# Kernel tuning notes

Measured on AMD Instinct MI355X. Metric: run time of the kernel, lower is better.

## Reference

```python
import jax, jax.numpy as jnp
import numpy as np

INTER = 32  # inter_channels = in_channels // 2


def conv1x1(x, w, b):
    # x: (b, c_in, h, w), w: (c_out, c_in), b: (c_out,)
    return jnp.einsum('bchw,oc->bohw', x, w) + b[None, :, None, None]


def setup_inputs() -> dict:
    key = jax.random.key(0)
    ks = jax.random.split(key, 12)
    B, C, H, W = 8, 64, 64, 64
    inter = INTER
    s_in = 1.0 / np.sqrt(C)      # torch conv default init scale
    s_int = 1.0 / np.sqrt(inter)
    return {
        'x': jax.random.normal(ks[0], (B, C, H, W), jnp.float32),
        'g_w': jax.random.normal(ks[1], (inter, C), jnp.float32) * s_in,
        'g_b': jax.random.normal(ks[2], (inter,), jnp.float32) * s_in,
        'theta_w': jax.random.normal(ks[3], (inter, C), jnp.float32) * s_in,
        'theta_b': jax.random.normal(ks[4], (inter,), jnp.float32) * s_in,
        'phi_w': jax.random.normal(ks[5], (inter, C), jnp.float32) * s_in,
        'phi_b': jax.random.normal(ks[6], (inter,), jnp.float32) * s_in,
        'W_w': jax.random.normal(ks[7], (C, inter), jnp.float32) * s_int,
        'W_b': jax.random.normal(ks[8], (C,), jnp.float32) * s_int,
        'Wz1_w': jax.random.normal(ks[9], (C, inter), jnp.float32) * s_int,
        'Wz1_b': jax.random.normal(ks[10], (C,), jnp.float32) * s_int,
        'mb': jax.random.normal(ks[11], (inter, 256), jnp.float32),
    }


def reference(x, g_w, g_b, theta_w, theta_b, phi_w, phi_b, W_w, W_b, Wz1_w, Wz1_b, mb):
    b, c, h, w = x.shape
    inter = g_w.shape[0]
    # 1x1 conv projections, flattened over spatial: N = h*w
    g_x = conv1x1(x, g_w, g_b).reshape(b, inter, -1)          # (b, ic, N)
    theta_x = conv1x1(x, theta_w, theta_b).reshape(b, inter, -1)
    phi_x = conv1x1(x, phi_w, phi_b).reshape(b, inter, -1)    # (b, ic, N)
    # non-local self-attention: f = theta^T @ phi, unscaled softmax
    f = jnp.einsum('bcn,bcm->bnm', theta_x, phi_x)            # (b, N, N)
    f_div_C = jax.nn.softmax(f, axis=-1)
    y = jnp.einsum('bnm,bcm->bcn', f_div_C, g_x)              # (b, ic, N)
    y = y.reshape(b, inter, h, w)
    W_y = conv1x1(y, W_w, W_b)                                # (b, c, h, w)
    # memory-bank cross-attention: phi^T @ mb, scaled softmax
    f1 = jnp.einsum('bcn,ck->bnk', phi_x, mb)                 # (b, N, 256)
    scale = jnp.float32(int(inter) ** (-0.5))
    f_div_C1 = jax.nn.softmax(f1 * scale, axis=-1)
    y1 = jnp.einsum('bnk,ck->bcn', f_div_C1, mb)              # (b, ic, N)
    y1 = y1.reshape(b, inter, h, w)
    W_y1 = conv1x1(y1, Wz1_w, Wz1_b)
    return W_y + x + W_y1
```

## Files before the change

### kernel.cpp

```cpp
#include <hip/hip_runtime.h>
#include <hip/hip_bf16.h>

#define N_POS 4096
#define C_IN 64
#define IC 32
#define L2E 1.4426950408889634f

typedef float f32x16 __attribute__((ext_vector_type(16)));
typedef short bf16x8 __attribute__((ext_vector_type(8)));
typedef unsigned int uint;
typedef uint uint4v __attribute__((ext_vector_type(4)));
typedef unsigned short ushort;

static __device__ __forceinline__ ushort f2bf(float f) {
    __hip_bfloat16 h = __float2bfloat16(f);
    return __builtin_bit_cast(ushort, h);
}
static __device__ __forceinline__ uint packbf2(float lo, float hi) {
    return (uint)f2bf(lo) | ((uint)f2bf(hi) << 16);
}
static __device__ __forceinline__ uint packtrunc(float lo, float hi) {
    return __builtin_amdgcn_perm(__builtin_bit_cast(uint, hi),
                                 __builtin_bit_cast(uint, lo), 0x07060302u);
}

__global__ __launch_bounds__(128) void proj_kernel(
    const float* __restrict__ x,
    const float* __restrict__ g_w, const float* __restrict__ g_b,
    const float* __restrict__ th_w, const float* __restrict__ th_b,
    const float* __restrict__ ph_w, const float* __restrict__ ph_b,
    const float* __restrict__ mb,
    ushort* __restrict__ gcn, ushort* __restrict__ tht, ushort* __restrict__ pht,
    ushort* __restrict__ mbt, ushort* __restrict__ mbb)
{
    int gy = blockIdx.y;
    int pj = gy >> 2, q8 = gy & 3;
    const float* wsrc = (pj == 0) ? g_w : (pj == 1) ? th_w : ph_w;
    const float* bsrc = (pj == 0) ? g_b : (pj == 1) ? th_b : ph_b;
    __shared__ float w[8][64];
    __shared__ float bias[8];
    int tid = threadIdx.x;
    for (int i = tid; i < 512; i += 128) w[i >> 6][i & 63] = wsrc[q8 * 512 + i];
    if (tid < 8) bias[tid] = bsrc[q8 * 8 + tid];
    __syncthreads();

    int ng = blockIdx.x * 128 + tid;
    int b = ng >> 12, n = ng & 4095;
    const float* xb = x + (size_t)b * C_IN * N_POS + n;
    float xr[64];
    #pragma unroll
    for (int c = 0; c < 64; c++) xr[c] = xb[(size_t)c * N_POS];

    float acc[8];
    #pragma unroll
    for (int o = 0; o < 8; o++) {
        float a = bias[o];
        const float4* w4 = (const float4*)w[o];
        #pragma unroll
        for (int c4 = 0; c4 < 16; c4++) {
            float4 wv = w4[c4];
            a += wv.x * xr[c4*4+0] + wv.y * xr[c4*4+1]
               + wv.z * xr[c4*4+2] + wv.w * xr[c4*4+3];
        }
        if (pj == 1) a *= L2E;
        acc[o] = a;
    }

    if (pj == 0) {
        #pragma unroll
        for (int c = 0; c < 8; c++)
            gcn[((size_t)(b * IC + q8 * 8 + c)) * N_POS + n] = f2bf(acc[c]);
    } else {
        ushort* dst = ((pj == 1) ? tht : pht) + ((size_t)(b * N_POS + n)) * IC + q8 * 8;
        uint4v pk;
        #pragma unroll
        for (int i = 0; i < 4; i++) pk[i] = packbf2(acc[2*i], acc[2*i+1]);
        *(uint4v*)dst = pk;
    }

    if (gy == 0 && blockIdx.x < 64) {
        int i = blockIdx.x * 128 + tid;
        int c = i >> 8, k = i & 255;
        float v = mb[i];
        mbb[i] = f2bf(v);
        mbt[k * 32 + c] = f2bf(v * (0.17677669529663687f * L2E));
    }
}

__global__ __launch_bounds__(512) void attn_fused(
    const ushort* __restrict__ tht, const ushort* __restrict__ pht,
    const ushort* __restrict__ gcn, const ushort* __restrict__ mbt,
    const ushort* __restrict__ mbb, const float* __restrict__ x,
    const float* __restrict__ Ww, const float* __restrict__ Wb,
    const float* __restrict__ Wzw, const float* __restrict__ Wzb,
    float* __restrict__ out)
{
    __shared__ float redY[4][2][32][36];
    __shared__ float redD[8][2][32];
    __shared__ float ly1p[4][32][36];
    __shared__ float sumeL[4][32];

    int tid = threadIdx.x;
    int s = tid >> 6, lane = tid & 63;
    int bid = blockIdx.x;
    int b = bid & 7;
    int qp = bid >> 3;
    int q0 = qp * 64;
    int mbase = s * 512;
    int cl = lane & 31, h = lane >> 5;
    int t4 = (cl >> 2) & 3;
    int pcl = (t4 == 1 || t4 == 2) ? (cl ^ 12) : cl;

    const ushort* thpA = tht + ((size_t)(b * N_POS + q0 + cl)) * IC + 8 * h;
    bf16x8 thA0 = *(const bf16x8*)thpA;
    bf16x8 thA1 = *(const bf16x8*)(thpA + 16);
    const ushort* thpB = thpA + 32 * IC;
    bf16x8 thB0 = *(const bf16x8*)thpB;
    bf16x8 thB1 = *(const bf16x8*)(thpB + 16);

    const ushort* phbase = pht + (size_t)b * N_POS * IC;
    const ushort* gbase  = gcn + ((size_t)(b * IC + cl)) * N_POS;

    f32x16 yA, yB, zero;
    #pragma unroll
    for (int i = 0; i < 16; i++) { yA[i] = 0.f; yB[i] = 0.f; zero[i] = 0.f; }
    float sA0 = 0.f, sA1 = 0.f, sB0 = 0.f, sB1 = 0.f;

    #pragma unroll 2
    for (int mt = 0; mt < 16; ++mt) {
        int m0 = mbase + mt * 32;
        const ushort* php = phbase + ((size_t)(m0 + pcl)) * IC + 8 * h;
        bf16x8 ph0 = *(const bf16x8*)php;
        bf16x8 ph1 = *(const bf16x8*)(php + 16);
        const ushort* gp = gbase + m0 + 8 * h;
        bf16x8 g0 = *(const bf16x8*)gp;
        bf16x8 g1 = *(const bf16x8*)(gp + 16);

        f32x16 sv = __builtin_amdgcn_mfma_f32_32x32x16_bf16(ph0, thA0, zero, 0, 0, 0);
        sv = __builtin_amdgcn_mfma_f32_32x32x16_bf16(ph1, thA1, sv, 0, 0, 0);
        uint wA[8];
        #pragma unroll
        for (int i = 0; i < 8; i++) {
            float p0 = __builtin_amdgcn_exp2f(sv[2*i]);
            float p1 = __builtin_amdgcn_exp2f(sv[2*i+1]);
            if (i & 1) sA1 += p0 + p1; else sA0 += p0 + p1;
            wA[i] = packtrunc(p0, p1);
        }
        f32x16 sw = __builtin_amdgcn_mfma_f32_32x32x16_bf16(ph0, thB0, zero, 0, 0, 0);
        sw = __builtin_amdgcn_mfma_f32_32x32x16_bf16(ph1, thB1, sw, 0, 0, 0);
        uint wB[8];
        #pragma unroll
        for (int i = 0; i < 8; i++) {
            float p0 = __builtin_amdgcn_exp2f(sw[2*i]);
            float p1 = __builtin_amdgcn_exp2f(sw[2*i+1]);
            if (i & 1) sB1 += p0 + p1; else sB0 += p0 + p1;
            wB[i] = packtrunc(p0, p1);
        }

        uint4v aA0, aA1, aB0, aB1;
        aA0[0] = wA[0]; aA0[1] = wA[1]; aA0[2] = wA[2]; aA0[3] = wA[3];
        aA1[0] = wA[4]; aA1[1] = wA[5]; aA1[2] = wA[6]; aA1[3] = wA[7];
        aB0[0] = wB[0]; aB0[1] = wB[1]; aB0[2] = wB[2]; aB0[3] = wB[3];
        aB1[0] = wB[4]; aB1[1] = wB[5]; aB1[2] = wB[6]; aB1[3] = wB[7];

        yA = __builtin_amdgcn_mfma_f32_32x32x16_bf16(
            __builtin_bit_cast(bf16x8, aA0), g0, yA, 0, 0, 0);
        yB = __builtin_amdgcn_mfma_f32_32x32x16_bf16(
            __builtin_bit_cast(bf16x8, aB0), g0, yB, 0, 0, 0);
        yA = __builtin_amdgcn_mfma_f32_32x32x16_bf16(
            __builtin_bit_cast(bf16x8, aA1), g1, yA, 0, 0, 0);
        yB = __builtin_amdgcn_mfma_f32_32x32x16_bf16(
            __builtin_bit_cast(bf16x8, aB1), g1, yB, 0, 0, 0);
    }

    float sumeA = sA0 + sA1;
    float sumeB = sB0 + sB1;

    sumeA += __shfl_xor(sumeA, 32);
    sumeB += __shfl_xor(sumeB, 32);
    if (lane < 32) { redD[s][0][cl] = sumeA; redD[s][1][cl] = sumeB; }
    if (s < 4) {
        #pragma unroll
        for (int r = 0; r < 16; r++) {
            int q = (r & 3) + 8 * (r >> 2) + 4 * h;
            redY[s][0][q][cl] = yA[r];
            redY[s][1][q][cl] = yB[r];
        }
    }
    __syncthreads();

    if (s >= 4) {
        int sl = s - 4;
        #pragma unroll
        for (int r = 0; r < 16; r++) {
            int q = (r & 3) + 8 * (r >> 2) + 4 * h;
            redY[sl][0][q][cl] += yA[r];
            redY[sl][1][q][cl] += yB[r];
        }
    } else {
        int j = s & 1, kh = s >> 1;
        int mq0 = q0 + j * 32;
        const ushort* php = pht + ((size_t)(b * N_POS + mq0 + cl)) * IC + 8 * h;
        bf16x8 qf0 = *(const bf16x8*)php;
        bf16x8 qf1 = *(const bf16x8*)(php + 16);

        yA = zero;
        yB = zero;
        float su0 = 0.f, su1 = 0.f;

        #pragma unroll
        for (int kt = 0; kt < 4; ++kt) {
            int k0 = (kh * 4 + kt) * 32;
            const ushort* ap = mbt + ((size_t)(k0 + pcl)) * IC + 8 * h;
            bf16x8 af0 = *(const bf16x8*)ap;
            bf16x8 af1 = *(const bf16x8*)(ap + 16);
            const ushort* bp = mbb + (size_t)cl * 256 + k0 + 8 * h;
            bf16x8 bf0 = *(const bf16x8*)bp;
            bf16x8 bf1 = *(const bf16x8*)(bp + 16);

            f32x16 sv = __builtin_amdgcn_mfma_f32_32x32x16_bf16(af0, qf0, zero, 0, 0, 0);
            sv = __builtin_amdgcn_mfma_f32_32x32x16_bf16(af1, qf1, sv, 0, 0, 0);

            uint w[8];
            #pragma unroll
            for (int i = 0; i < 8; i++) {
                float p0 = __builtin_amdgcn_exp2f(sv[2*i]);
                float p1 = __builtin_amdgcn_exp2f(sv[2*i+1]);
                if (i & 1) su1 += p0 + p1; else su0 += p0 + p1;
                w[i] = packtrunc(p0, p1);
            }
            uint4v a0, a1;
            a0[0] = w[0]; a0[1] = w[1]; a0[2] = w[2]; a0[3] = w[3];
            a1[0] = w[4]; a1[1] = w[5]; a1[2] = w[6]; a1[3] = w[7];

            yA = __builtin_amdgcn_mfma_f32_32x32x16_bf16(
                __builtin_bit_cast(bf16x8, a0), bf0, yA, 0, 0, 0);
            yB = __builtin_amdgcn_mfma_f32_32x32x16_bf16(
                __builtin_bit_cast(bf16x8, a1), bf1, yB, 0, 0, 0);
        }

        float sume = su0 + su1;
        sume += __shfl_xor(sume, 32);
        if (lane < 32) sumeL[s][cl] = sume;
        #pragma unroll
        for (int r = 0; r < 16; r++) {
            int q = (r & 3) + 8 * (r >> 2) + 4 * h;
            ly1p[s][q][cl] = yA[r] + yB[r];
        }
    }
    __syncthreads();

    int nl = lane, og = s;
    int n = q0 + nl;
    int jo = nl >> 5, qo = nl & 31;

    float den = 0.f;
    #pragma unroll
    for (int s8 = 0; s8 < 8; s8++) den += redD[s8][jo][qo];
    float inv = 1.f / den;
    float inv1 = 1.f / (sumeL[jo][qo] + sumeL[2 + jo][qo]);

    float yv[32], y1v[32];
    #pragma unroll
    for (int c4 = 0; c4 < 8; c4++) {
        float4 v0 = *(const float4*)&redY[0][jo][qo][c4 * 4];
        float4 v1 = *(const float4*)&redY[1][jo][qo][c4 * 4];
        float4 v2 = *(const float4*)&redY[2][jo][qo][c4 * 4];
        float4 v3 = *(const float4*)&redY[3][jo][qo][c4 * 4];
        yv[c4*4+0] = (v0.x + v1.x + v2.x + v3.x) * inv;
        yv[c4*4+1] = (v0.y + v1.y + v2.y + v3.y) * inv;
        yv[c4*4+2] = (v0.z + v1.z + v2.z + v3.z) * inv;
        yv[c4*4+3] = (v0.w + v1.w + v2.w + v3.w) * inv;
        float4 p0 = *(const float4*)&ly1p[jo][qo][c4 * 4];
        float4 p1 = *(const float4*)&ly1p[2 + jo][qo][c4 * 4];
        y1v[c4*4+0] = (p0.x + p1.x) * inv1;
        y1v[c4*4+1] = (p0.y + p1.y) * inv1;
        y1v[c4*4+2] = (p0.z + p1.z) * inv1;
        y1v[c4*4+3] = (p0.w + p1.w) * inv1;
    }

    int obase = og * 8;
    const float* xb = x   + ((size_t)(b * C_IN + obase)) * N_POS + n;
    float*       ob = out + ((size_t)(b * C_IN + obase)) * N_POS + n;
    #pragma unroll
    for (int o = 0; o < 8; o++) {
        float acc = Wb[obase + o] + Wzb[obase + o] + xb[(size_t)o * N_POS];
        const float4* w4  = (const float4*)(Ww  + (obase + o) * 32);
        const float4* wz4 = (const float4*)(Wzw + (obase + o) * 32);
        #pragma unroll
        for (int c4 = 0; c4 < 8; c4++) {
            float4 a = w4[c4], z = wz4[c4];
            acc += a.x * yv[c4*4+0] + a.y * yv[c4*4+1] + a.z * yv[c4*4+2] + a.w * yv[c4*4+3];
            acc += z.x * y1v[c4*4+0] + z.y * y1v[c4*4+1] + z.z * y1v[c4*4+2] + z.w * y1v[c4*4+3];
        }
        ob[(size_t)o * N_POS] = acc;
    }
}

extern "C" void kernel_launch(void* const* d_in, const int* in_sizes, int n_in,
                              void* d_out, int out_size, void* d_ws, size_t ws_size,
                              hipStream_t stream) {
    const float* x    = (const float*)d_in[0];
    const float* g_w  = (const float*)d_in[1];
    const float* g_b  = (const float*)d_in[2];
    const float* th_w = (const float*)d_in[3];
    const float* th_b = (const float*)d_in[4];
    const float* ph_w = (const float*)d_in[5];
    const float* ph_b = (const float*)d_in[6];
    const float* W_w  = (const float*)d_in[7];
    const float* W_b  = (const float*)d_in[8];
    const float* Wz_w = (const float*)d_in[9];
    const float* Wz_b = (const float*)d_in[10];
    const float* mb   = (const float*)d_in[11];
    float* out = (float*)d_out;

    char* w = (char*)d_ws;
    ushort* tht = (ushort*)w;
    ushort* pht = (ushort*)(w + (2u << 20));
    ushort* gcn = (ushort*)(w + (4u << 20));
    ushort* mbt = (ushort*)(w + (6u << 20));
    ushort* mbb = (ushort*)(w + (6u << 20) + 16384);

    proj_kernel<<<dim3(256, 12), 128, 0, stream>>>(x, g_w, g_b, th_w, th_b,
                                                   ph_w, ph_b, mb,
                                                   gcn, tht, pht, mbt, mbb);
    attn_fused<<<512, 512, 0, stream>>>(tht, pht, gcn, mbt, mbb, x,
                                        W_w, W_b, Wz_w, Wz_b, out);
}
```

Before: 74.02 us.

## Restructure projection kernel to compute all three projections per block with split-K

The projection kernel now has each block compute 48 output channels (16 each of g, theta, phi) for 64 positions. Four lanes split the 64 input channels and are combined with cross-lane shuffles. Before, twelve separate y-blocks each reloaded the full x column for only 8 outputs. The change is meant to cut redundant global reads of x (about sixfold fewer) and raise work per thread, at the cost of shuffle reductions, more registers for 48 accumulators, and only a quarter of lanes doing the stores.

```diff
diff --git a/kernel.cpp b/kernel.cpp
--- a/kernel.cpp
+++ b/kernel.cpp
@@ -24,7 +24,7 @@
                                  __builtin_bit_cast(uint, lo), 0x07060302u);
 }
 
-__global__ __launch_bounds__(128) void proj_kernel(
+__global__ __launch_bounds__(256) void proj_kernel(
     const float* __restrict__ x,
     const float* __restrict__ g_w, const float* __restrict__ g_b,
     const float* __restrict__ th_w, const float* __restrict__ th_b,
@@ -33,52 +33,88 @@
     ushort* __restrict__ gcn, ushort* __restrict__ tht, ushort* __restrict__ pht,
     ushort* __restrict__ mbt, ushort* __restrict__ mbb)
 {
-    int gy = blockIdx.y;
-    int pj = gy >> 2, q8 = gy & 3;
-    const float* wsrc = (pj == 0) ? g_w : (pj == 1) ? th_w : ph_w;
-    const float* bsrc = (pj == 0) ? g_b : (pj == 1) ? th_b : ph_b;
-    __shared__ float w[8][64];
-    __shared__ float bias[8];
+    int half = blockIdx.y;
+    __shared__ float w[48][64];
+    __shared__ float bias[48];
     int tid = threadIdx.x;
-    for (int i = tid; i < 512; i += 128) w[i >> 6][i & 63] = wsrc[q8 * 512 + i];
-    if (tid < 8) bias[tid] = bsrc[q8 * 8 + tid];
+    for (int i = tid; i < 3072; i += 256) {
+        int r = i >> 6, c = i & 63;
+        const float* src = (r < 16) ? g_w : (r < 32) ? th_w : ph_w;
+        float v = src[((r & 15) + half * 16) * 64 + c];
+        if (r >= 16 && r < 32) v *= L2E;
+        w[r][c] = v;
+    }
+    if (tid < 48) {
+        const float* bsrc = (tid < 16) ? g_b : (tid < 32) ? th_b : ph_b;
+        float v = bsrc[(tid & 15) + half * 16];
+        if (tid >= 16 && tid < 32) v *= L2E;
+        bias[tid] = v;
+    }
     __syncthreads();
 
-    int ng = blockIdx.x * 128 + tid;
-    int b = ng >> 12, n = ng & 4095;
-    const float* xb = x + (size_t)b * C_IN * N_POS + n;
-    float xr[64];
-    #pragma unroll
-    for (int c = 0; c < 64; c++) xr[c] = xb[(size_t)c * N_POS];
-
-    float acc[8];
-    #pragma unroll
-    for (int o = 0; o < 8; o++) {
-        float a = bias[o];
-        const float4* w4 = (const float4*)w[o];
-        #pragma unroll
-        for (int c4 = 0; c4 < 16; c4++) {
+    int ks = tid & 3;
+    int pos = blockIdx.x * 64 + (tid >> 2);
+    int b = pos >> 12, n = pos & 4095;
+    const float* xb = x + ((size_t)(b * C_IN + ks * 16)) * N_POS + n;
+    float xr[16];
+    #pragma unroll
+    for (int c = 0; c < 16; c++) xr[c] = xb[(size_t)c * N_POS];
+
+    float acc[48];
+    #pragma unroll
+    for (int o = 0; o < 48; o++) {
+        float a = 0.f;
+        const float4* w4 = (const float4*)&w[o][ks * 16];
+        #pragma unroll
+        for (int c4 = 0; c4 < 4; c4++) {
             float4 wv = w4[c4];
             a += wv.x * xr[c4*4+0] + wv.y * xr[c4*4+1]
                + wv.z * xr[c4*4+2] + wv.w * xr[c4*4+3];
         }
-        if (pj == 1) a *= L2E;
         acc[o] = a;
     }
-
-    if (pj == 0) {
-        #pragma unroll
-        for (int c = 0; c < 8; c++)
-            gcn[((size_t)(b * IC + q8 * 8 + c)) * N_POS + n] = f2bf(acc[c]);
-    } else {
-        ushort* dst = ((pj == 1) ? tht : pht) + ((size_t)(b * N_POS + n)) * IC + q8 * 8;
-        uint4v pk;
-        #pragma unroll
-        for (int i = 0; i < 4; i++) pk[i] = packbf2(acc[2*i], acc[2*i+1]);
-        *(uint4v*)dst = pk;
-    }
-
-    if (gy == 0 && blockIdx.x < 64) {
+    #pragma unroll
+    for (int o = 0; o < 48; o++) {
+        acc[o] += __shfl_xor(acc[o], 1);
+        acc[o] += __shfl_xor(acc[o], 2);
+    }
+
+    if (ks == 0) {
+        #pragma unroll
+        for (int c = 0; c < 16; c++)
+            gcn[((size_t)(b * IC + half * 16 + c)) * N_POS + n] =
+                f2bf(acc[c] + bias[c]);
+        {
+            ushort* dst = tht + ((size_t)(b * N_POS + n)) * IC + half * 16;
+            uint4v pk0, pk1;
+            #pragma unroll
+            for (int i = 0; i < 4; i++)
+                pk0[i] = packbf2(acc[16 + 2*i] + bias[16 + 2*i],
+                                 acc[17 + 2*i] + bias[17 + 2*i]);
+            #pragma unroll
+            for (int i = 0; i < 4; i++)
+                pk1[i] = packbf2(acc[24 + 2*i] + bias[24 + 2*i],
+                                 acc[25 + 2*i] + bias[25 + 2*i]);
+            *(uint4v*)dst = pk0;
+            *(uint4v*)(dst + 8) = pk1;
+        }
+        {
+            ushort* dst = pht + ((size_t)(b * N_POS + n)) * IC + half * 16;
+            uint4v pk0, pk1;
+            #pragma unroll
+            for (int i = 0; i < 4; i++)
+                pk0[i] = packbf2(acc[32 + 2*i] + bias[32 + 2*i],
+                                 acc[33 + 2*i] + bias[33 + 2*i]);
+            #pragma unroll
+            for (int i = 0; i < 4; i++)
+                pk1[i] = packbf2(acc[40 + 2*i] + bias[40 + 2*i],
+                                 acc[41 + 2*i] + bias[41 + 2*i]);
+            *(uint4v*)dst = pk0;
+            *(uint4v*)(dst + 8) = pk1;
+        }
+    }
+
+    if (half == 0 && blockIdx.x < 64 && tid < 128) {
         int i = blockIdx.x * 128 + tid;
         int c = i >> 8, k = i & 255;
         float v = mb[i];
@@ -321,9 +357,9 @@
     ushort* mbt = (ushort*)(w + (6u << 20));
     ushort* mbb = (ushort*)(w + (6u << 20) + 16384);
 
-    proj_kernel<<<dim3(256, 12), 128, 0, stream>>>(x, g_w, g_b, th_w, th_b,
-                                                   ph_w, ph_b, mb,
-                                                   gcn, tht, pht, mbt, mbb);
+    proj_kernel<<<dim3(512, 2), 256, 0, stream>>>(x, g_w, g_b, th_w, th_b,
+                                                  ph_w, ph_b, mb,
+                                                  gcn, tht, pht, mbt, mbb);
     attn_fused<<<512, 512, 0, stream>>>(tht, pht, gcn, mbt, mbb, x,
                                         W_w, W_b, Wz_w, Wz_b, out);
 }
```

Measured after the change: 83.41 us. +12.7%, slower.
